# Performance work log

Hardware: AMD Instinct MI355X
Metric: run time of the kernel (lower is better)

Reference implementation:

```python
import jax, jax.numpy as jnp
import numpy as np

EPS = 1e-5

def ste(x):
    # straight-through sign: forward = sign(x), backward = identity
    # (matches torch .data mutation trick in BinarizeConv2d/BinarizeLinear)
    return x + jax.lax.stop_gradient(jnp.sign(x) - x)

def conv(x, w, stride, pad):
    return jax.lax.conv_general_dilated(
        x, w, window_strides=stride,
        padding=[(pad[0], pad[0]), (pad[1], pad[1])],
        dimension_numbers=('NCHW', 'OIHW', 'NCHW'))

def bn2d(x, g, b):  # training-mode batch stats (module default .train())
    m = jnp.mean(x, axis=(0, 2, 3), keepdims=True)
    v = jnp.var(x, axis=(0, 2, 3), keepdims=True)
    return (x - m) * jax.lax.rsqrt(v + EPS) * g[None, :, None, None] + b[None, :, None, None]

def bn1d(x, g, b):
    m = jnp.mean(x, axis=0, keepdims=True)
    v = jnp.var(x, axis=0, keepdims=True)
    return (x - m) * jax.lax.rsqrt(v + EPS) * g[None, :] + b[None, :]

def prelu(x, a):
    return jnp.where(x >= 0, x, a * x)

def _forward(x, w1, w2, w3, w4, w5, w6, w7, w8, w9, w10,
             g1, b1, g2, b2, g3, b3, g4, b4, g5, b5,
             a1, a2, a3, a4, a5,
             fc1, fc2, fc3, g6, b6, g7, b7, a6, a7):
    h = x[:, None]  # (B,1,1100,9)
    # stage cfg: (wa,wb), bn, prelu, pad_a, (stride_b), bin_input flags
    stages = [
        ((w1, w2), (g1, b1), a1, (2, 0), (5, 1), (False, False)),
        ((w3, w4), (g2, b2), a2, (2, 0), (5, 1), (True, True)),
        ((w5, w6), (g3, b3), a3, (5, 0), (11, 1), (True, True)),
        ((w7, w8), (g4, b4), a4, (0, 1), (1, 3), (True, True)),
        ((w9, w10), (g5, b5), a5, (0, 1), (1, 3), (True, True)),
    ]
    for (wa, wb), (g, b), a, pad_a, stride_b, (bin_a, bin_b) in stages:
        if bin_a:
            h = ste(h)
        h = conv(h, ste(wa), (1, 1), pad_a)
        if bin_b:
            h = ste(h)
        h = conv(h, ste(wb), stride_b, (0, 0))
        h = prelu(bn2d(h, g, b), a)
    h = h.reshape(h.shape[0], -1)  # (B,1024)
    h = h @ ste(fc1).T                       # no input binarization (flag False)
    h = prelu(bn1d(h, g6, b6), a6)           # dropout skipped (eval/deterministic)
    h = ste(h) @ ste(fc2).T
    h = prelu(bn1d(h, g7, b7), a7)
    h = ste(h) @ ste(fc3).T                  # (B,2)
    return h

def setup_inputs() -> dict:
    key = jax.random.key(0)
    ks = jax.random.split(key, 20)
    C = [16, 32, 64, 128, 256]
    width = 0.01
    d = {'x': jax.random.normal(ks[0], (512, 1100, 9), jnp.float32)}
    shapes = [
        (C[0], 1, 5, 1), (C[0], C[0], 5, 1),
        (C[1], C[0], 5, 1), (C[1], C[1], 5, 1),
        (C[2], C[1], 11, 1), (C[2], C[2], 11, 1),
        (C[3], C[2], 1, 3), (C[3], C[3], 1, 3),
        (C[4], C[3], 1, 3), (C[4], C[4], 1, 3),
    ]
    for i, s in enumerate(shapes):
        d[f'w{i+1}'] = jax.random.normal(ks[1 + i], s, jnp.float32) * width
    for i, c in enumerate(C):
        d[f'g{i+1}'] = jnp.ones((c,), jnp.float32)
        d[f'b{i+1}'] = jnp.zeros((c,), jnp.float32)
        d[f'a{i+1}'] = jnp.asarray(0.25, jnp.float32)
    d['fc1'] = jax.random.uniform(ks[11], (256, 1024), jnp.float32, -width / 2, width / 2)
    d['fc2'] = jax.random.uniform(ks[12], (64, 256), jnp.float32, -width / 2, width / 2)
    d['fc3'] = jax.random.uniform(ks[13], (2, 64), jnp.float32, -width / 2, width / 2)
    d['g6'] = jnp.ones((256,), jnp.float32); d['b6'] = jnp.zeros((256,), jnp.float32)
    d['g7'] = jnp.ones((64,), jnp.float32); d['b7'] = jnp.zeros((64,), jnp.float32)
    d['a6'] = jnp.asarray(0.25, jnp.float32); d['a7'] = jnp.asarray(0.25, jnp.float32)
    return d

def reference(x, w1, w2, w3, w4, w5, w6, w7, w8, w9, w10,
              g1, b1, g2, b2, g3, b3, g4, b4, g5, b5,
              a1, a2, a3, a4, a5,
              fc1, fc2, fc3, g6, b6, g7, b7, a6, a7):
    return _forward(x, w1, w2, w3, w4, w5, w6, w7, w8, w9, w10,
                    g1, b1, g2, b2, g3, b3, g4, b4, g5, b5,
                    a1, a2, a3, a4, a5,
                    fc1, fc2, fc3, g6, b6, g7, b7, a6, a7)
```

## Files before the change

### kernel.cpp

```cpp
#include <hip/hip_runtime.h>
#include <hip/hip_bf16.h>

#define EPSV 1e-5

__device__ __forceinline__ float fsign(float x) {
    return (float)((x > 0.f) - (x < 0.f));
}

struct WPtrs {
    const float* src[3];
    float* dst[3];
    int n[3];
};

__global__ void sign_weights_kernel(WPtrs wp) {
    int wi = blockIdx.y;
    int n = wp.n[wi];
    const float* s = wp.src[wi];
    float* d = wp.dst[wi];
    for (int i = blockIdx.x * blockDim.x + threadIdx.x; i < n; i += gridDim.x * blockDim.x)
        d[i] = fsign(s[i]);
}

__global__ void build_wc_kernel(const float* __restrict__ w1, const float* __restrict__ w2,
                                float* __restrict__ wc) {
    int t = threadIdx.x;
    if (t < 208) {
        int co = t / 13, r = t % 13;
        float s = 0.f;
        for (int ci = 0; ci < 16; ++ci)
#pragma unroll
            for (int kh = 0; kh < 5; ++kh) {
                int k5 = r - kh;
                if (k5 >= 0 && k5 < 5)
                    s += fsign(w2[(co * 16 + ci) * 5 + kh]) * fsign(w1[ci * 5 + k5]);
            }
        wc[t] = s;
    }
}

struct PW { const float* src; unsigned* dnz; unsigned* dsg; int cout, cin, k, nw; };
struct PWall { PW l[8]; };

__global__ void pack_weights_kernel(PWall pa) {
    PW p = pa.l[blockIdx.y];
    int total = p.cout * p.k * p.nw;
    for (int u = blockIdx.x * blockDim.x + threadIdx.x; u < total; u += gridDim.x * blockDim.x) {
        int co = u / (p.k * p.nw);
        int rem = u % (p.k * p.nw);
        int kk = rem / p.nw, wi = rem % p.nw;
        unsigned nz = 0, sg = 0;
        for (int j = 0; j < 32; ++j) {
            int ci = wi * 32 + j;
            if (ci < p.cin) {
                float v = p.src[(co * p.cin + ci) * p.k + kk];
                if (v != 0.f) nz |= 1u << j;
                if (v < 0.f) sg |= 1u << j;
            }
        }
        p.dnz[u] = nz;
        p.dsg[u] = sg;
    }
}

__global__ void stage1_kernel(const float* __restrict__ x, const float* __restrict__ wcg,
                              float* __restrict__ p1) {
    int n = blockIdx.y;
    int ho0 = blockIdx.x * 28;
    int nrows = min(28, 220 - ho0);
    int nrx = 5 * nrows + 8;
    __shared__ float xs[148 * 9];
    __shared__ float wcl[208];
    int t = threadIdx.x;
    if (t < 208) wcl[t] = wcg[t];
    int hbase = 5 * ho0 - 2;
    for (int i = t; i < nrx * 9; i += 256) {
        int r = i / 9, w = i - r * 9, h = hbase + r;
        xs[i] = (h >= 0 && h < 1100) ? x[(n * 1100 + h) * 9 + w] : 0.f;
    }
    __syncthreads();
    int npos = nrows * 9;
    if (t < npos) {
        int hoL = t / 9, w = t - hoL * 9;
        double xr[13];
        int base = 45 * hoL + w;
#pragma unroll
        for (int r = 0; r < 13; ++r) xr[r] = (double)xs[base + 9 * r];
        int ho = ho0 + hoL;
        long obase = ((long)n * 16) * 1980 + ho * 9 + w;
#pragma unroll
        for (int co = 0; co < 16; ++co) {
            double acc = 0.0;
#pragma unroll
            for (int r = 0; r < 13; ++r)
                acc += (double)wcl[co * 13 + r] * xr[r];
            p1[obase + co * 1980] = (float)acc;
        }
    }
}

__global__ void stats_rows(const float* __restrict__ x, int C, int N, int HW, int S,
                           double* __restrict__ part) {
    int c = blockIdx.x, s = blockIdx.y;
    int nlo = (int)((long)N * s / S), nhi = (int)((long)N * (s + 1) / S);
    unsigned HW4 = (unsigned)HW >> 2;
    unsigned tot = (unsigned)(nhi - nlo) * HW4;
    double sum = 0, sq = 0;
    for (unsigned u = threadIdx.x; u < tot; u += 256) {
        unsigned nn = u / HW4, j = u - nn * HW4;
        const float4 v = ((const float4*)(x + ((long)((nlo + nn) * C + c)) * HW))[j];
        sum += v.x; sq += (double)v.x * v.x;
        sum += v.y; sq += (double)v.y * v.y;
        sum += v.z; sq += (double)v.z * v.z;
        sum += v.w; sq += (double)v.w * v.w;
    }
    __shared__ double ls[256], lq[256];
    ls[threadIdx.x] = sum;
    lq[threadIdx.x] = sq;
    __syncthreads();
    for (int off = 128; off > 0; off >>= 1) {
        if ((int)threadIdx.x < off) {
            ls[threadIdx.x] += ls[threadIdx.x + off];
            lq[threadIdx.x] += lq[threadIdx.x + off];
        }
        __syncthreads();
    }
    if (threadIdx.x == 0) {
        part[(c * S + s) * 2] = ls[0];
        part[(c * S + s) * 2 + 1] = lq[0];
    }
}

__global__ void stats_final(const double* __restrict__ part, int C, int S, long count,
                            float* __restrict__ mean, float* __restrict__ rstd) {
    int c = blockIdx.x * blockDim.x + threadIdx.x;
    if (c >= C) return;
    double s = 0, q = 0;
    for (int i = 0; i < S; ++i) {
        s += part[(c * S + i) * 2];
        q += part[(c * S + i) * 2 + 1];
    }
    double m = s / (double)count;
    double v = q / (double)count - m * m;
    mean[c] = (float)m;
    rstd[c] = (float)(1.0 / sqrt(v + EPSV));
}

__global__ void stats_bn1d(const float* __restrict__ x, int C, int N,
                           float* __restrict__ mean, float* __restrict__ rstd) {
    int c = blockIdx.x;
    double sum = 0, sq = 0;
    for (int n = threadIdx.x; n < N; n += 64) {
        float v = x[(long)n * C + c];
        sum += v;
        sq += (double)v * v;
    }
    for (int off = 32; off > 0; off >>= 1) {
        sum += __shfl_down(sum, off);
        sq += __shfl_down(sq, off);
    }
    if (threadIdx.x == 0) {
        double m = sum / (double)N;
        double v = sq / (double)N - m * m;
        mean[c] = (float)m;
        rstd[c] = (float)(1.0 / sqrt(v + EPSV));
    }
}

__global__ void stage2_kernel(const float* __restrict__ p1, const float* __restrict__ mean,
    const float* __restrict__ rstd, const float* __restrict__ g, const float* __restrict__ b,
    const float* __restrict__ ap, const unsigned* __restrict__ w3n, const unsigned* __restrict__ w3s,
    const unsigned* __restrict__ w4n, const unsigned* __restrict__ w4s, float* __restrict__ p2) {
    int hb = blockIdx.x;
    int n = blockIdx.y;
    float a = ap[0];
    __shared__ __align__(16) uint2 qx[216];
    __shared__ __align__(16) uint2 ax[180];
    __shared__ __align__(16) uint2 w3L[160];
    __shared__ __align__(16) uint2 w4L[160];
    int t = threadIdx.x;
    if (t < 160) {
        int kh = t / 32, co = t % 32;
        w3L[t] = make_uint2(w3n[co * 5 + kh], w3s[co * 5 + kh]);
        w4L[t] = make_uint2(w4n[t], w4s[t]);
    }
    if (t < 216) {
        int rl = t / 9, w = t % 9;
        int r = 20 * hb - 2 + rl;
        unsigned nz = 0, sg = 0;
        if (r >= 0 && r < 220) {
            for (int ci = 0; ci < 16; ++ci) {
                float v = p1[(n * 16 + ci) * 1980 + r * 9 + w];
                float bnv = (v - mean[ci]) * rstd[ci] * g[ci] + b[ci];
                float pr = bnv < 0.f ? a * bnv : bnv;
                if (pr != 0.f) { nz |= 1u << ci; if (pr < 0.f) sg |= 1u << ci; }
            }
        }
        qx[t] = make_uint2(nz, sg);
    }
    __syncthreads();
    if (t < 180) {
        int jl = t / 9, w = t % 9;
        uint2 xv[5];
#pragma unroll
        for (int kh = 0; kh < 5; ++kh) xv[kh] = qx[(jl + kh) * 9 + w];
        unsigned onz = 0, osg = 0;
        for (int co = 0; co < 32; co += 2) {
            int c0 = 0, n0 = 0, c1 = 0, n1 = 0;
#pragma unroll
            for (int kh = 0; kh < 5; ++kh) {
                const uint4 wv = *(const uint4*)&w3L[kh * 32 + co];
                unsigned b0 = xv[kh].x & wv.x;
                c0 += __popc(b0);
                n0 += __popc((xv[kh].y ^ wv.y) & b0);
                unsigned b1 = xv[kh].x & wv.z;
                c1 += __popc(b1);
                n1 += __popc((xv[kh].y ^ wv.w) & b1);
            }
            int s0 = c0 - 2 * n0, s1 = c1 - 2 * n1;
            if (s0 != 0) { onz |= 1u << co; if (s0 < 0) osg |= 1u << co; }
            if (s1 != 0) { onz |= 1u << (co + 1); if (s1 < 0) osg |= 1u << (co + 1); }
        }
        ax[t] = make_uint2(onz, osg);
    }
    __syncthreads();
    for (int o = t; o < 1152; o += 256) {
        int co = o / 36, rem = o % 36, hol = rem / 9, w = rem % 9;
        int cnt = 0, neg = 0;
#pragma unroll
        for (int kh = 0; kh < 5; ++kh) {
            uint2 av = ax[(5 * hol + kh) * 9 + w];
            uint2 wv = w4L[co * 5 + kh];
            unsigned both = av.x & wv.x;
            cnt += __popc(both);
            neg += __popc((av.y ^ wv.y) & both);
        }
        p2[(n * 32 + co) * 396 + (4 * hb + hol) * 9 + w] = (float)(cnt - 2 * neg);
    }
}

__global__ void stage3_kernel(const float* __restrict__ p2, const float* __restrict__ mean,
    const float* __restrict__ rstd, const float* __restrict__ g, const float* __restrict__ b,
    const float* __restrict__ ap, const unsigned* __restrict__ w5n, const unsigned* __restrict__ w5s,
    const unsigned* __restrict__ w6n, const unsigned* __restrict__ w6s, float* __restrict__ p3) {
    int ho = blockIdx.x;
    int n = blockIdx.y;
    float a = ap[0];
    __shared__ __align__(16) uint2 qx[189];
    __shared__ __align__(16) uint2 ax[99 * 2];
    __shared__ __align__(16) uint2 w5L[704];
    __shared__ __align__(16) uint2 w6L[1408];
    int t = threadIdx.x;
    for (int i = t; i < 704; i += 256) {
        int kh = i / 64, co = i % 64;
        w5L[i] = make_uint2(w5n[co * 11 + kh], w5s[co * 11 + kh]);
    }
    for (int i = t; i < 1408; i += 256)
        w6L[i] = make_uint2(w6n[i], w6s[i]);
    if (t < 189) {
        int rl = t / 9, w = t % 9;
        int r = 11 * ho - 5 + rl;
        unsigned nz = 0, sg = 0;
        if (r >= 0 && r < 44) {
            for (int ci = 0; ci < 32; ++ci) {
                float v = p2[(n * 32 + ci) * 396 + r * 9 + w];
                float bnv = (v - mean[ci]) * rstd[ci] * g[ci] + b[ci];
                float pr = bnv < 0.f ? a * bnv : bnv;
                if (pr != 0.f) { nz |= 1u << ci; if (pr < 0.f) sg |= 1u << ci; }
            }
        }
        qx[t] = make_uint2(nz, sg);
    }
    __syncthreads();
    if (t < 198) {
        int p = t >> 1, wi = t & 1;
        int jl = p / 9, w = p % 9;
        uint2 xv[11];
#pragma unroll
        for (int kh = 0; kh < 11; ++kh) xv[kh] = qx[(jl + kh) * 9 + w];
        unsigned onz = 0, osg = 0;
        for (int jj = 0; jj < 32; jj += 2) {
            int co0 = wi * 32 + jj;
            int c0 = 0, n0 = 0, c1 = 0, n1 = 0;
#pragma unroll
            for (int kh = 0; kh < 11; ++kh) {
                const uint4 wv = *(const uint4*)&w5L[kh * 64 + co0];
                unsigned b0 = xv[kh].x & wv.x;
                c0 += __popc(b0);
                n0 += __popc((xv[kh].y ^ wv.y) & b0);
                unsigned b1 = xv[kh].x & wv.z;
                c1 += __popc(b1);
                n1 += __popc((xv[kh].y ^ wv.w) & b1);
            }
            int s0 = c0 - 2 * n0, s1 = c1 - 2 * n1;
            if (s0 != 0) { onz |= 1u << jj; if (s0 < 0) osg |= 1u << jj; }
            if (s1 != 0) { onz |= 1u << (jj + 1); if (s1 < 0) osg |= 1u << (jj + 1); }
        }
        ax[p * 2 + wi] = make_uint2(onz, osg);
    }
    __syncthreads();
    for (int o = t; o < 576; o += 256) {
        int co = o / 9, w = o % 9;
        int cA = 0, nA = 0, cB = 0, nB = 0;
        for (int kh = 0; kh < 11; ++kh) {
            const uint4 av = *(const uint4*)&ax[(kh * 9 + w) * 2];
            const uint4 wv = *(const uint4*)&w6L[(co * 11 + kh) * 2];
            unsigned b0 = av.x & wv.x;
            cA += __popc(b0);
            nA += __popc((av.y ^ wv.y) & b0);
            unsigned b1 = av.z & wv.z;
            cB += __popc(b1);
            nB += __popc((av.w ^ wv.w) & b1);
        }
        p3[(n * 64 + co) * 36 + ho * 9 + w] = (float)((cA + cB) - 2 * (nA + nB));
    }
}

__global__ void stage4_kernel(const float* __restrict__ p3, const float* __restrict__ mean,
    const float* __restrict__ rstd, const float* __restrict__ g, const float* __restrict__ b,
    const float* __restrict__ ap, const unsigned* __restrict__ w7n, const unsigned* __restrict__ w7s,
    const unsigned* __restrict__ w8n, const unsigned* __restrict__ w8s, float* __restrict__ p4) {
    int h = blockIdx.x;
    int n = blockIdx.y;
    float a = ap[0];
    __shared__ unsigned q[9 * 4];
    __shared__ signed char strit[9 * 128];
    __shared__ unsigned an[9 * 4], ag[9 * 4];
    int t = threadIdx.x;
    if (t < 18) {
        int w = t >> 1, half = t & 1;
        unsigned nz = 0, sg = 0;
        for (int j = 0; j < 32; ++j) {
            int ci = half * 32 + j;
            float v = p3[(n * 64 + ci) * 36 + h * 9 + w];
            float bnv = (v - mean[ci]) * rstd[ci] * g[ci] + b[ci];
            float pr = bnv < 0.f ? a * bnv : bnv;
            if (pr != 0.f) { nz |= 1u << j; if (pr < 0.f) sg |= 1u << j; }
        }
        q[w * 4 + half] = nz; q[w * 4 + 2 + half] = sg;
    }
    __syncthreads();
    for (int o = t; o < 1152; o += 256) {
        int w = o / 128, co = o % 128;
        int cnt = 0, neg = 0;
        for (int kw = 0; kw < 3; ++kw) {
            int wl = w + kw - 1;
            if (wl < 0 || wl >= 9) continue;
#pragma unroll
            for (int iw = 0; iw < 2; ++iw) {
                unsigned both = q[wl * 4 + iw] & w7n[(co * 3 + kw) * 2 + iw];
                cnt += __popc(both);
                neg += __popc((q[wl * 4 + 2 + iw] ^ w7s[(co * 3 + kw) * 2 + iw]) & both);
            }
        }
        int s = cnt - 2 * neg;
        strit[o] = (signed char)((s > 0) - (s < 0));
    }
    __syncthreads();
    if (t < 36) {
        int w = t >> 2, wi = t & 3;
        unsigned nz = 0, sg = 0;
        for (int j = 0; j < 32; ++j) {
            int tr = strit[w * 128 + wi * 32 + j];
            if (tr) { nz |= 1u << j; if (tr < 0) sg |= 1u << j; }
        }
        an[w * 4 + wi] = nz; ag[w * 4 + wi] = sg;
    }
    __syncthreads();
    for (int o = t; o < 384; o += 256) {
        int co = o / 3, wo = o % 3;
        int cnt = 0, neg = 0;
        for (int kw = 0; kw < 3; ++kw) {
            int wl = 3 * wo + kw;
#pragma unroll
            for (int iw = 0; iw < 4; ++iw) {
                unsigned both = an[wl * 4 + iw] & w8n[(co * 3 + kw) * 4 + iw];
                cnt += __popc(both);
                neg += __popc((ag[wl * 4 + iw] ^ w8s[(co * 3 + kw) * 4 + iw]) & both);
            }
        }
        p4[(n * 128 + co) * 12 + h * 3 + wo] = (float)(cnt - 2 * neg);
    }
}

__global__ void stage5_kernel(const float* __restrict__ p4, const float* __restrict__ mean,
    const float* __restrict__ rstd, const float* __restrict__ g, const float* __restrict__ b,
    const float* __restrict__ ap, const unsigned* __restrict__ w9n, const unsigned* __restrict__ w9s,
    const unsigned* __restrict__ w10n, const unsigned* __restrict__ w10s, float* __restrict__ p5) {
    int h = blockIdx.x;
    int n = blockIdx.y;
    float a = ap[0];
    __shared__ unsigned q[3 * 8];
    __shared__ signed char strit[3 * 256];
    __shared__ unsigned an[3 * 8], ag[3 * 8];
    int t = threadIdx.x;
    if (t < 12) {
        int w = t >> 2, wq = t & 3;
        unsigned nz = 0, sg = 0;
        for (int j = 0; j < 32; ++j) {
            int ci = wq * 32 + j;
            float v = p4[(n * 128 + ci) * 12 + h * 3 + w];
            float bnv = (v - mean[ci]) * rstd[ci] * g[ci] + b[ci];
            float pr = bnv < 0.f ? a * bnv : bnv;
            if (pr != 0.f) { nz |= 1u << j; if (pr < 0.f) sg |= 1u << j; }
        }
        q[w * 8 + wq] = nz; q[w * 8 + 4 + wq] = sg;
    }
    __syncthreads();
    for (int o = t; o < 768; o += 256) {
        int w = o / 256, co = o % 256;
        int cnt = 0, neg = 0;
        for (int kw = 0; kw < 3; ++kw) {
            int wl = w + kw - 1;
            if (wl < 0 || wl >= 3) continue;
#pragma unroll
            for (int iw = 0; iw < 4; ++iw) {
                unsigned both = q[wl * 8 + iw] & w9n[(co * 3 + kw) * 4 + iw];
                cnt += __popc(both);
                neg += __popc((q[wl * 8 + 4 + iw] ^ w9s[(co * 3 + kw) * 4 + iw]) & both);
            }
        }
        int s = cnt - 2 * neg;
        strit[o] = (signed char)((s > 0) - (s < 0));
    }
    __syncthreads();
    if (t < 24) {
        int w = t >> 3, wi = t & 7;
        unsigned nz = 0, sg = 0;
        for (int j = 0; j < 32; ++j) {
            int tr = strit[w * 256 + wi * 32 + j];
            if (tr) { nz |= 1u << j; if (tr < 0) sg |= 1u << j; }
        }
        an[w * 8 + wi] = nz; ag[w * 8 + wi] = sg;
    }
    __syncthreads();
    if (t < 256) {
        int co = t;
        int cnt = 0, neg = 0;
        for (int kw = 0; kw < 3; ++kw) {
#pragma unroll
            for (int iw = 0; iw < 8; ++iw) {
                unsigned both = an[kw * 8 + iw] & w10n[(co * 3 + kw) * 8 + iw];
                cnt += __popc(both);
                neg += __popc((ag[kw * 8 + iw] ^ w10s[(co * 3 + kw) * 8 + iw]) & both);
            }
        }
        p5[n * 1024 + co * 4 + h] = (float)(cnt - 2 * neg);
    }
}

__global__ void fc1_kernel(const float* __restrict__ p5, const float* __restrict__ mean,
                           const float* __restrict__ rstd, const float* __restrict__ g,
                           const float* __restrict__ b, const float* __restrict__ ap,
                           const float* __restrict__ sfc1, float* __restrict__ h1) {
    int n = blockIdx.x;
    float a = ap[0];
    __shared__ float hv[1024];
    int t = threadIdx.x;
    for (int idx = t; idx < 1024; idx += 256) {
        int c = idx >> 2;
        float v = p5[n * 1024 + idx];
        float bnv = (v - mean[c]) * rstd[c] * g[c] + b[c];
        hv[idx] = bnv < 0.f ? a * bnv : bnv;
    }
    __syncthreads();
    int wave = t >> 6, lane = t & 63;
    float hr[16];
#pragma unroll
    for (int m = 0; m < 16; ++m) hr[m] = hv[lane * 16 + m];
    for (int jj = 0; jj < 64; ++jj) {
        int j = wave * 64 + jj;
        const float4* wr = (const float4*)(sfc1 + (j << 10) + (lane << 4));
        double s = 0.0;
#pragma unroll
        for (int q4 = 0; q4 < 4; ++q4) {
            float4 wv = wr[q4];
            s += (double)(hr[q4 * 4 + 0] * wv.x);
            s += (double)(hr[q4 * 4 + 1] * wv.y);
            s += (double)(hr[q4 * 4 + 2] * wv.z);
            s += (double)(hr[q4 * 4 + 3] * wv.w);
        }
#pragma unroll
        for (int off = 32; off > 0; off >>= 1) s += __shfl_down(s, off, 64);
        if (lane == 0) h1[n * 256 + j] = (float)s;
    }
}

__global__ void fc2_kernel(const float* __restrict__ h1, const float* __restrict__ mean,
                           const float* __restrict__ rstd, const float* __restrict__ g,
                           const float* __restrict__ b, const float* __restrict__ ap,
                           const float* __restrict__ sfc2, float* __restrict__ h2) {
    int n = blockIdx.x;
    float a = ap[0];
    __shared__ float sv[256];
    int t = threadIdx.x;
    if (t < 256) {
        float v = h1[n * 256 + t];
        float bnv = (v - mean[t]) * rstd[t] * g[t] + b[t];
        float pr = bnv < 0.f ? a * bnv : bnv;
        sv[t] = fsign(pr);
    }
    __syncthreads();
    if (t < 64) {
        float s = 0.f;
        for (int k = 0; k < 256; ++k) s += sv[k] * sfc2[t * 256 + k];
        h2[n * 64 + t] = s;
    }
}

__global__ void fc3_kernel(const float* __restrict__ h2, const float* __restrict__ mean,
                           const float* __restrict__ rstd, const float* __restrict__ g,
                           const float* __restrict__ b, const float* __restrict__ ap,
                           const float* __restrict__ sfc3, float* __restrict__ out) {
    int n = blockIdx.x;
    float a = ap[0];
    __shared__ float sv[64];
    int t = threadIdx.x;
    if (t < 64) {
        float v = h2[n * 64 + t];
        float bnv = (v - mean[t]) * rstd[t] * g[t] + b[t];
        float pr = bnv < 0.f ? a * bnv : bnv;
        sv[t] = fsign(pr);
    }
    __syncthreads();
    if (t < 2) {
        float s = 0.f;
        for (int k = 0; k < 64; ++k) s += sv[k] * sfc3[t * 64 + k];
        out[n * 2 + t] = s;
    }
}

extern "C" void kernel_launch(void* const* d_in, const int* in_sizes, int n_in,
                              void* d_out, int out_size, void* d_ws, size_t ws_size,
                              hipStream_t stream) {
    const float* x = (const float*)d_in[0];
    const float* G[8] = {nullptr, (const float*)d_in[11], (const float*)d_in[14],
                         (const float*)d_in[17], (const float*)d_in[20], (const float*)d_in[23],
                         (const float*)d_in[29], (const float*)d_in[31]};
    const float* B[8] = {nullptr, (const float*)d_in[12], (const float*)d_in[15],
                         (const float*)d_in[18], (const float*)d_in[21], (const float*)d_in[24],
                         (const float*)d_in[30], (const float*)d_in[32]};
    const float* A[8] = {nullptr, (const float*)d_in[13], (const float*)d_in[16],
                         (const float*)d_in[19], (const float*)d_in[22], (const float*)d_in[25],
                         (const float*)d_in[33], (const float*)d_in[34]};

    float* ws = (float*)d_ws;
    size_t off = 0;
    const int fsz[3] = {262144, 16384, 128};
    float* fw[3];
    for (int i = 0; i < 3; ++i) { fw[i] = ws + off; off += (size_t)fsz[i]; }
    float* sfc1 = fw[0]; float* sfc2 = fw[1]; float* sfc3 = fw[2];
    float* wc = ws + off; off += 208;

    const int psz[8] = {160, 160, 704, 1408, 768, 1536, 3072, 6144};
    unsigned* pn[8]; unsigned* pg[8];
    for (int i = 0; i < 8; ++i) {
        pn[i] = (unsigned*)(ws + off); off += (size_t)psz[i];
        pg[i] = (unsigned*)(ws + off); off += (size_t)psz[i];
    }

    float* p1 = ws + off; off += 16220160;
    float* p2 = ws + off; off += 6488064;
    float* p3 = ws + off; off += 1179648;
    float* p4 = ws + off; off += 786432;
    float* p5 = ws + off; off += 524288;
    float* h1 = ws + off; off += 131072;
    float* h2 = ws + off; off += 32768;
    float* mean1 = ws + off; off += 16;  float* rstd1 = ws + off; off += 16;
    float* mean2 = ws + off; off += 32;  float* rstd2 = ws + off; off += 32;
    float* mean3 = ws + off; off += 64;  float* rstd3 = ws + off; off += 64;
    float* mean4 = ws + off; off += 128; float* rstd4 = ws + off; off += 128;
    float* mean5 = ws + off; off += 256; float* rstd5 = ws + off; off += 256;
    float* mean6 = ws + off; off += 256; float* rstd6 = ws + off; off += 256;
    float* mean7 = ws + off; off += 64;  float* rstd7 = ws + off; off += 64;
    if (off & 1) off += 1;
    double* part = (double*)(ws + off); off += 2 * 16384;

    WPtrs wp;
    const int fsrc_idx[3] = {26, 27, 28};
    for (int i = 0; i < 3; ++i) {
        wp.src[i] = (const float*)d_in[fsrc_idx[i]];
        wp.dst[i] = fw[i];
        wp.n[i] = fsz[i];
    }
    hipLaunchKernelGGL(sign_weights_kernel, dim3(32, 3), dim3(256), 0, stream, wp);
    hipLaunchKernelGGL(build_wc_kernel, dim3(1), dim3(256), 0, stream,
                       (const float*)d_in[1], (const float*)d_in[2], wc);

    PWall pa;
    const int cout_[8] = {32, 32, 64, 64, 128, 128, 256, 256};
    const int cin_[8]  = {16, 32, 32, 64, 64, 128, 128, 256};
    const int kk_[8]   = {5, 5, 11, 11, 3, 3, 3, 3};
    for (int i = 0; i < 8; ++i) {
        pa.l[i].src = (const float*)d_in[3 + i];
        pa.l[i].dnz = pn[i];
        pa.l[i].dsg = pg[i];
        pa.l[i].cout = cout_[i];
        pa.l[i].cin = cin_[i];
        pa.l[i].k = kk_[i];
        pa.l[i].nw = (cin_[i] + 31) / 32;
    }
    hipLaunchKernelGGL(pack_weights_kernel, dim3(4, 8), dim3(256), 0, stream, pa);

    hipLaunchKernelGGL(stage1_kernel, dim3(8, 512), dim3(256), 0, stream, x, wc, p1);
    hipLaunchKernelGGL(stats_rows, dim3(16, 64), dim3(256), 0, stream, p1, 16, 512, 1980, 64, part);
    hipLaunchKernelGGL(stats_final, dim3(1), dim3(256), 0, stream, part, 16, 64, (long)512 * 1980, mean1, rstd1);

    hipLaunchKernelGGL(stage2_kernel, dim3(11, 512), dim3(256), 0, stream, p1, mean1, rstd1,
                       G[1], B[1], A[1], pn[0], pg[0], pn[1], pg[1], p2);
    hipLaunchKernelGGL(stats_rows, dim3(32, 64), dim3(256), 0, stream, p2, 32, 512, 396, 64, part);
    hipLaunchKernelGGL(stats_final, dim3(1), dim3(256), 0, stream, part, 32, 64, (long)512 * 396, mean2, rstd2);

    hipLaunchKernelGGL(stage3_kernel, dim3(4, 512), dim3(256), 0, stream, p2, mean2, rstd2,
                       G[2], B[2], A[2], pn[2], pg[2], pn[3], pg[3], p3);
    hipLaunchKernelGGL(stats_rows, dim3(64, 16), dim3(256), 0, stream, p3, 64, 512, 36, 16, part);
    hipLaunchKernelGGL(stats_final, dim3(1), dim3(256), 0, stream, part, 64, 16, (long)512 * 36, mean3, rstd3);

    hipLaunchKernelGGL(stage4_kernel, dim3(4, 512), dim3(256), 0, stream, p3, mean3, rstd3,
                       G[3], B[3], A[3], pn[4], pg[4], pn[5], pg[5], p4);
    hipLaunchKernelGGL(stats_rows, dim3(128, 16), dim3(256), 0, stream, p4, 128, 512, 12, 16, part);
    hipLaunchKernelGGL(stats_final, dim3(1), dim3(256), 0, stream, part, 128, 16, (long)512 * 12, mean4, rstd4);

    hipLaunchKernelGGL(stage5_kernel, dim3(4, 512), dim3(256), 0, stream, p4, mean4, rstd4,
                       G[4], B[4], A[4], pn[6], pg[6], pn[7], pg[7], p5);
    hipLaunchKernelGGL(stats_rows, dim3(256, 8), dim3(256), 0, stream, p5, 256, 512, 4, 8, part);
    hipLaunchKernelGGL(stats_final, dim3(1), dim3(256), 0, stream, part, 256, 8, (long)512 * 4, mean5, rstd5);

    hipLaunchKernelGGL(fc1_kernel, dim3(512), dim3(256), 0, stream, p5, mean5, rstd5,
                       G[5], B[5], A[5], sfc1, h1);
    hipLaunchKernelGGL(stats_bn1d, dim3(256), dim3(64), 0, stream, h1, 256, 512, mean6, rstd6);

    hipLaunchKernelGGL(fc2_kernel, dim3(512), dim3(256), 0, stream, h1, mean6, rstd6,
                       G[6], B[6], A[6], sfc2, h2);
    hipLaunchKernelGGL(stats_bn1d, dim3(64), dim3(64), 0, stream, h2, 64, 512, mean7, rstd7);

    hipLaunchKernelGGL(fc3_kernel, dim3(512), dim3(256), 0, stream, h2, mean7, rstd7,
                       G[7], B[7], A[7], sfc3, (float*)d_out);
}
```

Before: 332.1 us.

## Fuse BN statistics into conv stages and switch intermediates to channels-last layout

Each conv stage now reduces per-channel sum and sum-of-squares for its own output tile and writes per-block partials, so the separate stats_rows pass that re-read every intermediate activation is gone. A parallel per-channel finalize kernel replaces the single-block serial finalize. Intermediates move to channel-innermost layout so the next stage reads each position's channels with float4 loads. The cost is a much larger partials buffer, extra shared memory and reductions inside each stage, and shuffle reductions in stage1.

```diff
diff --git a/kernel.cpp b/kernel.cpp
--- a/kernel.cpp
+++ b/kernel.cpp
@@ -63,87 +63,29 @@
     }
 }
 
-__global__ void stage1_kernel(const float* __restrict__ x, const float* __restrict__ wcg,
-                              float* __restrict__ p1) {
-    int n = blockIdx.y;
-    int ho0 = blockIdx.x * 28;
-    int nrows = min(28, 220 - ho0);
-    int nrx = 5 * nrows + 8;
-    __shared__ float xs[148 * 9];
-    __shared__ float wcl[208];
-    int t = threadIdx.x;
-    if (t < 208) wcl[t] = wcg[t];
-    int hbase = 5 * ho0 - 2;
-    for (int i = t; i < nrx * 9; i += 256) {
-        int r = i / 9, w = i - r * 9, h = hbase + r;
-        xs[i] = (h >= 0 && h < 1100) ? x[(n * 1100 + h) * 9 + w] : 0.f;
-    }
-    __syncthreads();
-    int npos = nrows * 9;
-    if (t < npos) {
-        int hoL = t / 9, w = t - hoL * 9;
-        double xr[13];
-        int base = 45 * hoL + w;
-#pragma unroll
-        for (int r = 0; r < 13; ++r) xr[r] = (double)xs[base + 9 * r];
-        int ho = ho0 + hoL;
-        long obase = ((long)n * 16) * 1980 + ho * 9 + w;
-#pragma unroll
-        for (int co = 0; co < 16; ++co) {
-            double acc = 0.0;
-#pragma unroll
-            for (int r = 0; r < 13; ++r)
-                acc += (double)wcl[co * 13 + r] * xr[r];
-            p1[obase + co * 1980] = (float)acc;
-        }
-    }
-}
-
-__global__ void stats_rows(const float* __restrict__ x, int C, int N, int HW, int S,
-                           double* __restrict__ part) {
-    int c = blockIdx.x, s = blockIdx.y;
-    int nlo = (int)((long)N * s / S), nhi = (int)((long)N * (s + 1) / S);
-    unsigned HW4 = (unsigned)HW >> 2;
-    unsigned tot = (unsigned)(nhi - nlo) * HW4;
-    double sum = 0, sq = 0;
-    for (unsigned u = threadIdx.x; u < tot; u += 256) {
-        unsigned nn = u / HW4, j = u - nn * HW4;
-        const float4 v = ((const float4*)(x + ((long)((nlo + nn) * C + c)) * HW))[j];
-        sum += v.x; sq += (double)v.x * v.x;
-        sum += v.y; sq += (double)v.y * v.y;
-        sum += v.z; sq += (double)v.z * v.z;
-        sum += v.w; sq += (double)v.w * v.w;
+__global__ void stats_finalp(const double* __restrict__ part, int S, long count,
+                             float* __restrict__ mean, float* __restrict__ rstd) {
+    int c = blockIdx.x, t = threadIdx.x;
+    int chunk = (S + 255) / 256;
+    int lo = t * chunk, hi = min(S, lo + chunk);
+    double s = 0, q = 0;
+    for (int i = lo; i < hi; ++i) {
+        s += part[((long)c * S + i) * 2];
+        q += part[((long)c * S + i) * 2 + 1];
     }
     __shared__ double ls[256], lq[256];
-    ls[threadIdx.x] = sum;
-    lq[threadIdx.x] = sq;
+    ls[t] = s; lq[t] = q;
     __syncthreads();
     for (int off = 128; off > 0; off >>= 1) {
-        if ((int)threadIdx.x < off) {
-            ls[threadIdx.x] += ls[threadIdx.x + off];
-            lq[threadIdx.x] += lq[threadIdx.x + off];
-        }
+        if (t < off) { ls[t] += ls[t + off]; lq[t] += lq[t + off]; }
         __syncthreads();
     }
-    if (threadIdx.x == 0) {
-        part[(c * S + s) * 2] = ls[0];
-        part[(c * S + s) * 2 + 1] = lq[0];
-    }
-}
-
-__global__ void stats_final(const double* __restrict__ part, int C, int S, long count,
-                            float* __restrict__ mean, float* __restrict__ rstd) {
-    int c = blockIdx.x * blockDim.x + threadIdx.x;
-    if (c >= C) return;
-    double s = 0, q = 0;
-    for (int i = 0; i < S; ++i) {
-        s += part[(c * S + i) * 2];
-        q += part[(c * S + i) * 2 + 1];
-    }
-    double m = s / (double)count;
-    double v = q / (double)count - m * m;
-    mean[c] = (float)m;
-    rstd[c] = (float)(1.0 / sqrt(v + EPSV));
+    if (t == 0) {
+        double m = ls[0] / (double)count;
+        double v = lq[0] / (double)count - m * m;
+        mean[c] = (float)m;
+        rstd[c] = (float)(1.0 / sqrt(v + EPSV));
+    }
 }
 
 __global__ void stats_bn1d(const float* __restrict__ x, int C, int N,
@@ -167,10 +109,74 @@
     }
 }
 
+__global__ void stage1_kernel(const float* __restrict__ x, const float* __restrict__ wcg,
+                              float* __restrict__ p1, double* __restrict__ part) {
+    int n = blockIdx.y;
+    int hb = blockIdx.x;
+    int ho0 = hb * 28;
+    int nrows = min(28, 220 - ho0);
+    int nrx = 5 * nrows + 8;
+    __shared__ float xs[148 * 9];
+    __shared__ float wcl[208];
+    __shared__ double sS[4 * 16], sQ[4 * 16];
+    int t = threadIdx.x;
+    if (t < 208) wcl[t] = wcg[t];
+    int hbase = 5 * ho0 - 2;
+    for (int i = t; i < nrx * 9; i += 256) {
+        int r = i / 9, w = i - r * 9, h = hbase + r;
+        xs[i] = (h >= 0 && h < 1100) ? x[(n * 1100 + h) * 9 + w] : 0.f;
+    }
+    __syncthreads();
+    int npos = nrows * 9;
+    bool act = t < npos;
+    float pv[16];
+    if (act) {
+        int hoL = t / 9, w = t - hoL * 9;
+        double xr[13];
+        int base = 45 * hoL + w;
+#pragma unroll
+        for (int r = 0; r < 13; ++r) xr[r] = (double)xs[base + 9 * r];
+#pragma unroll
+        for (int co = 0; co < 16; ++co) {
+            double acc = 0.0;
+#pragma unroll
+            for (int r = 0; r < 13; ++r)
+                acc += (double)wcl[co * 13 + r] * xr[r];
+            pv[co] = (float)acc;
+        }
+        int ho = ho0 + hoL;
+        float4* dst = (float4*)(p1 + (((long)n * 1980 + ho * 9 + w) << 4));
+#pragma unroll
+        for (int q4 = 0; q4 < 4; ++q4)
+            dst[q4] = make_float4(pv[q4 * 4], pv[q4 * 4 + 1], pv[q4 * 4 + 2], pv[q4 * 4 + 3]);
+    }
+    int lane = t & 63, wid = t >> 6;
+#pragma unroll
+    for (int co = 0; co < 16; ++co) {
+        double v = act ? (double)pv[co] : 0.0;
+        double vv = v * v;
+#pragma unroll
+        for (int off = 32; off > 0; off >>= 1) {
+            v += __shfl_down(v, off, 64);
+            vv += __shfl_down(vv, off, 64);
+        }
+        if (lane == 0) { sS[wid * 16 + co] = v; sQ[wid * 16 + co] = vv; }
+    }
+    __syncthreads();
+    if (t < 16) {
+        double s = sS[t] + sS[16 + t] + sS[32 + t] + sS[48 + t];
+        double q = sQ[t] + sQ[16 + t] + sQ[32 + t] + sQ[48 + t];
+        long blk = (long)n * 8 + hb;
+        part[((long)t * 4096 + blk) * 2] = s;
+        part[((long)t * 4096 + blk) * 2 + 1] = q;
+    }
+}
+
 __global__ void stage2_kernel(const float* __restrict__ p1, const float* __restrict__ mean,
     const float* __restrict__ rstd, const float* __restrict__ g, const float* __restrict__ b,
     const float* __restrict__ ap, const unsigned* __restrict__ w3n, const unsigned* __restrict__ w3s,
-    const unsigned* __restrict__ w4n, const unsigned* __restrict__ w4s, float* __restrict__ p2) {
+    const unsigned* __restrict__ w4n, const unsigned* __restrict__ w4s, float* __restrict__ p2,
+    double* __restrict__ part) {
     int hb = blockIdx.x;
     int n = blockIdx.y;
     float a = ap[0];
@@ -178,6 +184,7 @@
     __shared__ __align__(16) uint2 ax[180];
     __shared__ __align__(16) uint2 w3L[160];
     __shared__ __align__(16) uint2 w4L[160];
+    __shared__ float sArr[1152];
     int t = threadIdx.x;
     if (t < 160) {
         int kh = t / 32, co = t % 32;
@@ -189,9 +196,14 @@
         int r = 20 * hb - 2 + rl;
         unsigned nz = 0, sg = 0;
         if (r >= 0 && r < 220) {
+            const float4* src = (const float4*)(p1 + (((long)n * 1980 + r * 9 + w) << 4));
+            float4 v4[4];
+#pragma unroll
+            for (int q4 = 0; q4 < 4; ++q4) v4[q4] = src[q4];
+            const float* vals = (const float*)v4;
+#pragma unroll
             for (int ci = 0; ci < 16; ++ci) {
-                float v = p1[(n * 16 + ci) * 1980 + r * 9 + w];
-                float bnv = (v - mean[ci]) * rstd[ci] * g[ci] + b[ci];
+                float bnv = (vals[ci] - mean[ci]) * rstd[ci] * g[ci] + b[ci];
                 float pr = bnv < 0.f ? a * bnv : bnv;
                 if (pr != 0.f) { nz |= 1u << ci; if (pr < 0.f) sg |= 1u << ci; }
             }
@@ -225,7 +237,8 @@
     }
     __syncthreads();
     for (int o = t; o < 1152; o += 256) {
-        int co = o / 36, rem = o % 36, hol = rem / 9, w = rem % 9;
+        int pos = o >> 5, co = o & 31;
+        int hol = pos / 9, w = pos % 9;
         int cnt = 0, neg = 0;
 #pragma unroll
         for (int kh = 0; kh < 5; ++kh) {
@@ -235,14 +248,28 @@
             cnt += __popc(both);
             neg += __popc((av.y ^ wv.y) & both);
         }
-        p2[(n * 32 + co) * 396 + (4 * hb + hol) * 9 + w] = (float)(cnt - 2 * neg);
+        float val = (float)(cnt - 2 * neg);
+        sArr[o] = val;
+        p2[(((long)n * 396 + (4 * hb + hol) * 9 + w) << 5) + co] = val;
+    }
+    __syncthreads();
+    if (t < 32) {
+        double s = 0, q = 0;
+        for (int pos = 0; pos < 36; ++pos) {
+            double v = (double)sArr[pos * 32 + t];
+            s += v; q += v * v;
+        }
+        long blk = (long)hb * 512 + n;
+        part[((long)t * 5632 + blk) * 2] = s;
+        part[((long)t * 5632 + blk) * 2 + 1] = q;
     }
 }
 
 __global__ void stage3_kernel(const float* __restrict__ p2, const float* __restrict__ mean,
     const float* __restrict__ rstd, const float* __restrict__ g, const float* __restrict__ b,
     const float* __restrict__ ap, const unsigned* __restrict__ w5n, const unsigned* __restrict__ w5s,
-    const unsigned* __restrict__ w6n, const unsigned* __restrict__ w6s, float* __restrict__ p3) {
+    const unsigned* __restrict__ w6n, const unsigned* __restrict__ w6s, float* __restrict__ p3,
+    double* __restrict__ part) {
     int ho = blockIdx.x;
     int n = blockIdx.y;
     float a = ap[0];
@@ -250,6 +277,7 @@
     __shared__ __align__(16) uint2 ax[99 * 2];
     __shared__ __align__(16) uint2 w5L[704];
     __shared__ __align__(16) uint2 w6L[1408];
+    __shared__ float sArr[576];
     int t = threadIdx.x;
     for (int i = t; i < 704; i += 256) {
         int kh = i / 64, co = i % 64;
@@ -262,9 +290,14 @@
         int r = 11 * ho - 5 + rl;
         unsigned nz = 0, sg = 0;
         if (r >= 0 && r < 44) {
+            const float4* src = (const float4*)(p2 + (((long)n * 396 + r * 9 + w) << 5));
+            float4 v4[8];
+#pragma unroll
+            for (int q4 = 0; q4 < 8; ++q4) v4[q4] = src[q4];
+            const float* vals = (const float*)v4;
+#pragma unroll
             for (int ci = 0; ci < 32; ++ci) {
-                float v = p2[(n * 32 + ci) * 396 + r * 9 + w];
-                float bnv = (v - mean[ci]) * rstd[ci] * g[ci] + b[ci];
+                float bnv = (vals[ci] - mean[ci]) * rstd[ci] * g[ci] + b[ci];
                 float pr = bnv < 0.f ? a * bnv : bnv;
                 if (pr != 0.f) { nz |= 1u << ci; if (pr < 0.f) sg |= 1u << ci; }
             }
@@ -300,7 +333,7 @@
     }
     __syncthreads();
     for (int o = t; o < 576; o += 256) {
-        int co = o / 9, w = o % 9;
+        int co = o & 63, w = o >> 6;
         int cA = 0, nA = 0, cB = 0, nB = 0;
         for (int kh = 0; kh < 11; ++kh) {
             const uint4 av = *(const uint4*)&ax[(kh * 9 + w) * 2];
@@ -312,28 +345,48 @@
             cB += __popc(b1);
             nB += __popc((av.w ^ wv.w) & b1);
         }
-        p3[(n * 64 + co) * 36 + ho * 9 + w] = (float)((cA + cB) - 2 * (nA + nB));
+        float val = (float)((cA + cB) - 2 * (nA + nB));
+        sArr[o] = val;
+        p3[(((long)n * 36 + ho * 9 + w) << 6) + co] = val;
+    }
+    __syncthreads();
+    if (t < 64) {
+        double s = 0, q = 0;
+        for (int w = 0; w < 9; ++w) {
+            double v = (double)sArr[w * 64 + t];
+            s += v; q += v * v;
+        }
+        long blk = (long)ho * 512 + n;
+        part[((long)t * 2048 + blk) * 2] = s;
+        part[((long)t * 2048 + blk) * 2 + 1] = q;
     }
 }
 
 __global__ void stage4_kernel(const float* __restrict__ p3, const float* __restrict__ mean,
     const float* __restrict__ rstd, const float* __restrict__ g, const float* __restrict__ b,
     const float* __restrict__ ap, const unsigned* __restrict__ w7n, const unsigned* __restrict__ w7s,
-    const unsigned* __restrict__ w8n, const unsigned* __restrict__ w8s, float* __restrict__ p4) {
+    const unsigned* __restrict__ w8n, const unsigned* __restrict__ w8s, float* __restrict__ p4,
+    double* __restrict__ part) {
     int h = blockIdx.x;
     int n = blockIdx.y;
     float a = ap[0];
     __shared__ unsigned q[9 * 4];
     __shared__ signed char strit[9 * 128];
     __shared__ unsigned an[9 * 4], ag[9 * 4];
+    __shared__ float sArr[384];
     int t = threadIdx.x;
     if (t < 18) {
         int w = t >> 1, half = t & 1;
+        const float4* src = (const float4*)(p3 + (((long)n * 36 + h * 9 + w) << 6) + half * 32);
+        float4 v4[8];
+#pragma unroll
+        for (int q4 = 0; q4 < 8; ++q4) v4[q4] = src[q4];
+        const float* vals = (const float*)v4;
         unsigned nz = 0, sg = 0;
+#pragma unroll
         for (int j = 0; j < 32; ++j) {
             int ci = half * 32 + j;
-            float v = p3[(n * 64 + ci) * 36 + h * 9 + w];
-            float bnv = (v - mean[ci]) * rstd[ci] * g[ci] + b[ci];
+            float bnv = (vals[j] - mean[ci]) * rstd[ci] * g[ci] + b[ci];
             float pr = bnv < 0.f ? a * bnv : bnv;
             if (pr != 0.f) { nz |= 1u << j; if (pr < 0.f) sg |= 1u << j; }
         }
@@ -368,7 +421,7 @@
     }
     __syncthreads();
     for (int o = t; o < 384; o += 256) {
-        int co = o / 3, wo = o % 3;
+        int wo = o >> 7, co = o & 127;
         int cnt = 0, neg = 0;
         for (int kw = 0; kw < 3; ++kw) {
             int wl = 3 * wo + kw;
@@ -379,14 +432,28 @@
                 neg += __popc((ag[wl * 4 + iw] ^ w8s[(co * 3 + kw) * 4 + iw]) & both);
             }
         }
-        p4[(n * 128 + co) * 12 + h * 3 + wo] = (float)(cnt - 2 * neg);
+        float val = (float)(cnt - 2 * neg);
+        sArr[o] = val;
+        p4[(((long)n * 12 + h * 3 + wo) << 7) + co] = val;
+    }
+    __syncthreads();
+    if (t < 128) {
+        double s = 0, qd = 0;
+        for (int wo = 0; wo < 3; ++wo) {
+            double v = (double)sArr[wo * 128 + t];
+            s += v; qd += v * v;
+        }
+        long blk = (long)h * 512 + n;
+        part[((long)t * 2048 + blk) * 2] = s;
+        part[((long)t * 2048 + blk) * 2 + 1] = qd;
     }
 }
 
 __global__ void stage5_kernel(const float* __restrict__ p4, const float* __restrict__ mean,
     const float* __restrict__ rstd, const float* __restrict__ g, const float* __restrict__ b,
     const float* __restrict__ ap, const unsigned* __restrict__ w9n, const unsigned* __restrict__ w9s,
-    const unsigned* __restrict__ w10n, const unsigned* __restrict__ w10s, float* __restrict__ p5) {
+    const unsigned* __restrict__ w10n, const unsigned* __restrict__ w10s, float* __restrict__ p5,
+    double* __restrict__ part) {
     int h = blockIdx.x;
     int n = blockIdx.y;
     float a = ap[0];
@@ -396,11 +463,16 @@
     int t = threadIdx.x;
     if (t < 12) {
         int w = t >> 2, wq = t & 3;
+        const float4* src = (const float4*)(p4 + (((long)n * 12 + h * 3 + w) << 7) + wq * 32);
+        float4 v4[8];
+#pragma unroll
+        for (int q4 = 0; q4 < 8; ++q4) v4[q4] = src[q4];
+        const float* vals = (const float*)v4;
         unsigned nz = 0, sg = 0;
+#pragma unroll
         for (int j = 0; j < 32; ++j) {
             int ci = wq * 32 + j;
-            float v = p4[(n * 128 + ci) * 12 + h * 3 + w];
-            float bnv = (v - mean[ci]) * rstd[ci] * g[ci] + b[ci];
+            float bnv = (vals[j] - mean[ci]) * rstd[ci] * g[ci] + b[ci];
             float pr = bnv < 0.f ? a * bnv : bnv;
             if (pr != 0.f) { nz |= 1u << j; if (pr < 0.f) sg |= 1u << j; }
         }
@@ -445,7 +517,12 @@
                 neg += __popc((ag[kw * 8 + iw] ^ w10s[(co * 3 + kw) * 8 + iw]) & both);
             }
         }
-        p5[n * 1024 + co * 4 + h] = (float)(cnt - 2 * neg);
+        float val = (float)(cnt - 2 * neg);
+        p5[(long)n * 1024 + co * 4 + h] = val;
+        long blk = (long)h * 512 + n;
+        double v = (double)val;
+        part[((long)co * 2048 + blk) * 2] = v;
+        part[((long)co * 2048 + blk) * 2 + 1] = v * v;
     }
 }
 
@@ -574,7 +651,7 @@
     float* mean6 = ws + off; off += 256; float* rstd6 = ws + off; off += 256;
     float* mean7 = ws + off; off += 64;  float* rstd7 = ws + off; off += 64;
     if (off & 1) off += 1;
-    double* part = (double*)(ws + off); off += 2 * 16384;
+    double* part = (double*)(ws + off); off += 2 * 1048576;
 
     WPtrs wp;
     const int fsrc_idx[3] = {26, 27, 28};
@@ -602,29 +679,29 @@
     }
     hipLaunchKernelGGL(pack_weights_kernel, dim3(4, 8), dim3(256), 0, stream, pa);
 
-    hipLaunchKernelGGL(stage1_kernel, dim3(8, 512), dim3(256), 0, stream, x, wc, p1);
-    hipLaunchKernelGGL(stats_rows, dim3(16, 64), dim3(256), 0, stream, p1, 16, 512, 1980, 64, part);
-    hipLaunchKernelGGL(stats_final, dim3(1), dim3(256), 0, stream, part, 16, 64, (long)512 * 1980, mean1, rstd1);
+    hipLaunchKernelGGL(stage1_kernel, dim3(8, 512), dim3(256), 0, stream, x, wc, p1, part);
+    hipLaunchKernelGGL(stats_finalp, dim3(16), dim3(256), 0, stream, part, 4096,
+                       (long)512 * 1980, mean1, rstd1);
 
     hipLaunchKernelGGL(stage2_kernel, dim3(11, 512), dim3(256), 0, stream, p1, mean1, rstd1,
-                       G[1], B[1], A[1], pn[0], pg[0], pn[1], pg[1], p2);
-    hipLaunchKernelGGL(stats_rows, dim3(32, 64), dim3(256), 0, stream, p2, 32, 512, 396, 64, part);
-    hipLaunchKernelGGL(stats_final, dim3(1), dim3(256), 0, stream, part, 32, 64, (long)512 * 396, mean2, rstd2);
+                       G[1], B[1], A[1], pn[0], pg[0], pn[1], pg[1], p2, part);
+    hipLaunchKernelGGL(stats_finalp, dim3(32), dim3(256), 0, stream, part, 5632,
+                       (long)512 * 396, mean2, rstd2);
 
     hipLaunchKernelGGL(stage3_kernel, dim3(4, 512), dim3(256), 0, stream, p2, mean2, rstd2,
-                       G[2], B[2], A[2], pn[2], pg[2], pn[3], pg[3], p3);
-    hipLaunchKernelGGL(stats_rows, dim3(64, 16), dim3(256), 0, stream, p3, 64, 512, 36, 16, part);
-    hipLaunchKernelGGL(stats_final, dim3(1), dim3(256), 0, stream, part, 64, 16, (long)512 * 36, mean3, rstd3);
+                       G[2], B[2], A[2], pn[2], pg[2], pn[3], pg[3], p3, part);
+    hipLaunchKernelGGL(stats_finalp, dim3(64), dim3(256), 0, stream, part, 2048,
+                       (long)512 * 36, mean3, rstd3);
 
     hipLaunchKernelGGL(stage4_kernel, dim3(4, 512), dim3(256), 0, stream, p3, mean3, rstd3,
-                       G[3], B[3], A[3], pn[4], pg[4], pn[5], pg[5], p4);
-    hipLaunchKernelGGL(stats_rows, dim3(128, 16), dim3(256), 0, stream, p4, 128, 512, 12, 16, part);
-    hipLaunchKernelGGL(stats_final, dim3(1), dim3(256), 0, stream, part, 128, 16, (long)512 * 12, mean4, rstd4);
+                       G[3], B[3], A[3], pn[4], pg[4], pn[5], pg[5], p4, part);
+    hipLaunchKernelGGL(stats_finalp, dim3(128), dim3(256), 0, stream, part, 2048,
+                       (long)512 * 12, mean4, rstd4);
 
     hipLaunchKernelGGL(stage5_kernel, dim3(4, 512), dim3(256), 0, stream, p4, mean4, rstd4,
-                       G[4], B[4], A[4], pn[6], pg[6], pn[7], pg[7], p5);
-    hipLaunchKernelGGL(stats_rows, dim3(256, 8), dim3(256), 0, stream, p5, 256, 512, 4, 8, part);
-    hipLaunchKernelGGL(stats_final, dim3(1), dim3(256), 0, stream, part, 256, 8, (long)512 * 4, mean5, rstd5);
+                       G[4], B[4], A[4], pn[6], pg[6], pn[7], pg[7], p5, part);
+    hipLaunchKernelGGL(stats_finalp, dim3(256), dim3(256), 0, stream, part, 2048,
+                       (long)512 * 4, mean5, rstd5);
 
     hipLaunchKernelGGL(fc1_kernel, dim3(512), dim3(256), 0, stream, p5, mean5, rstd5,
                        G[5], B[5], A[5], sfc1, h1);
```

After: 351.2 us. 1.06x slower.
